# Optimization experiments

Hardware: AMD Instinct MI355X
Metric: run time of the kernel (lower is better)

Reference implementation:

```python
import jax, jax.numpy as jnp
from jax import lax
import numpy as np

B, S, T = 1024, 512, 48


def setup_inputs() -> dict:
    key = jax.random.key(0)
    k1, k2, k3, k4, k5, k6 = jax.random.split(key, 6)
    emissions = jax.random.normal(k1, (B, S, T), dtype=jnp.float32)
    tags = jax.random.randint(k2, (B, S), 0, T, dtype=jnp.int32)
    # variable-length mask; length >= 1 so position 0 is always valid
    lengths = jax.random.randint(k3, (B,), 1, S + 1, dtype=jnp.int32)
    mask = (jnp.arange(S)[None, :] < lengths[:, None]).astype(jnp.float32)
    transitions = jax.random.normal(k4, (T, T), dtype=jnp.float32)
    start_transitions = jax.random.normal(k5, (T,), dtype=jnp.float32)
    end_transitions = jax.random.normal(k6, (T,), dtype=jnp.float32)
    return {
        "emissions": emissions,
        "tags": tags,
        "mask": mask,
        "transitions": transitions,
        "start_transitions": start_transitions,
        "end_transitions": end_transitions,
    }


def _gold_score(emissions, tags, mask, transitions, start_transitions, end_transitions):
    # score of the gold tag sequence (vectorized over time)
    score = start_transitions[tags[:, 0]]
    score = score + jnp.take_along_axis(emissions[:, 0], tags[:, 0:1], axis=1)[:, 0]
    # NOTE: original code indexes transitions[cur_tag, prev_tag] here (faithful)
    trans_sc = transitions[tags[:, 1:], tags[:, :-1]]                      # [B, S-1]
    emit_sc = jnp.take_along_axis(emissions[:, 1:], tags[:, 1:, None], axis=2)[..., 0]
    score = score + jnp.sum((trans_sc + emit_sc) * mask[:, 1:], axis=1)
    seq_last = mask.sum(axis=1).astype(jnp.int32) - 1                      # [B]
    last_tags = jnp.take_along_axis(tags, seq_last[:, None], axis=1)[:, 0]
    return score + end_transitions[last_tags]


def _forward_algorithm(emissions, mask, transitions, start_transitions, end_transitions):
    # log-partition via logsumexp recurrence, lax.scan over time
    init = start_transitions[None, :] + emissions[:, 0]                    # [B, T]

    def step(score, xs):
        em_i, m_i = xs                                                     # [B,T], [B]
        # next[b, cur] = logsumexp_prev(score[b,prev] + trans[prev,cur] + em[b,cur])
        ns = jax.nn.logsumexp(score[:, :, None] + transitions[None] + em_i[:, None, :], axis=1)
        score = jnp.where(m_i[:, None] > 0, ns, score)
        return score, None

    xs = (jnp.swapaxes(emissions[:, 1:], 0, 1), jnp.swapaxes(mask[:, 1:], 0, 1))
    score, _ = lax.scan(step, init, xs)
    return jax.nn.logsumexp(score + end_transitions[None, :], axis=1)      # [B]


def reference(emissions, tags, mask, transitions, start_transitions, end_transitions):
    gold = _gold_score(emissions, tags, mask, transitions, start_transitions, end_transitions)
    fwd = _forward_algorithm(emissions, mask, transitions, start_transitions, end_transitions)
    return (fwd - gold).mean()
```

## Files before the change

### kernel.cpp

```cpp
#include <hip/hip_runtime.h>


#define T 48
#define SLEN 512
#define BATCH 1024

typedef _Float16 h2 __attribute__((ext_vector_type(2)));
typedef _Float16 h8v __attribute__((ext_vector_type(8)));
typedef h8v h8 __attribute__((may_alias));
typedef _Float16 f16ma __attribute__((may_alias));

__device__ __forceinline__ float wave_sum(float v) {
    #pragma unroll
    for (int m = 32; m >= 1; m >>= 1) v += __shfl_xor(v, m, 64);
    return v;
}
__device__ __forceinline__ float wave_max(float v) {
    #pragma unroll
    for (int m = 32; m >= 1; m >>= 1) v = fmaxf(v, __shfl_xor(v, m, 64));
    return v;
}
__device__ __forceinline__ float rlane(float v, int k) {
    return __int_as_float(__builtin_amdgcn_readlane(__float_as_int(v), k));
}
__device__ __forceinline__ float fdot2(h2 a, h2 b, float c) {
#if __has_builtin(__builtin_amdgcn_fdot2)
    return __builtin_amdgcn_fdot2(a, b, c, false);
#else
    return fmaf((float)a[1], (float)b[1], fmaf((float)a[0], (float)b[0], c));
#endif
}

#define H2OF(q, i) (__builtin_shufflevector((q), (q), 2*(i), 2*(i)+1))
#define DOTG(q, E, base, A0, A1, A2, A3)        \
    A0 = fdot2(H2OF(q,0), E[(base)+0], A0);     \
    A1 = fdot2(H2OF(q,1), E[(base)+1], A1);     \
    A2 = fdot2(H2OF(q,2), E[(base)+2], A2);     \
    A3 = fdot2(H2OF(q,3), E[(base)+3], A3);
#define DOT48(E, A0, A1, A2, A3, Q0,Q1,Q2,Q3,Q4,Q5) \
    DOTG(Q0, E, 0,  A0,A1,A2,A3)                \
    DOTG(Q1, E, 4,  A0,A1,A2,A3)                \
    DOTG(Q2, E, 8,  A0,A1,A2,A3)                \
    DOTG(Q3, E, 12, A0,A1,A2,A3)                \
    DOTG(Q4, E, 16, A0,A1,A2,A3)                \
    DOTG(Q5, E, 20, A0,A1,A2,A3)

__global__ __launch_bounds__(64) void crf_kernel(
    const float* __restrict__ em,
    const int*   __restrict__ tags,
    const float* __restrict__ mask,
    const float* __restrict__ trans,
    const float* __restrict__ start_t,
    const float* __restrict__ end_t,
    float*       __restrict__ out)
{
    constexpr float LOG2E = 1.4426950408889634f;
    constexpr float LN2   = 0.6931471805599453f;
    constexpr float ESC   = -8.0f;

    const int b    = blockIdx.x;
    const int lane = threadIdx.x;
    const int j    = lane < T ? lane : (T - 1);

    const float* em_b   = em   + (size_t)b * SLEN * T;
    const float* mask_b = mask + (size_t)b * SLEN;
    const int*   tags_b = tags + (size_t)b * SLEN;

    __shared__ __align__(16) _Float16 bufF[64];
    __shared__ __align__(16) _Float16 bufB[64];
    f16ma* wF = (f16ma*)bufF;
    f16ma* wB = (f16ma*)bufB;
    const h8* F8 = (const h8*)bufF;
    const h8* B8 = (const h8*)bufB;

    float msum = 0.f;
    for (int s = lane; s < SLEN; s += 64) msum += mask_b[s];
    msum = wave_sum(msum);
    const int len = (int)(msum + 0.5f);
    const int nb  = (len - 1) >> 1;
    const int nf  = (len - 1) - nb;

    float g = 0.f;
    for (int i = lane; i < len; i += 64) {
        if (i >= 1) {
            const int tc = tags_b[i];
            const int tp = tags_b[i - 1];
            g += trans[tc * T + tp] + em_b[(size_t)i * T + tc];
        }
    }
    g = wave_sum(g);

    h2 Ec[24], Er[24];
    #pragma unroll
    for (int k = 0; k < T; k += 2) {
        h2 c, r;
        c[0] = (_Float16)exp2f(trans[(k    ) * T + j] * LOG2E + ESC);
        c[1] = (_Float16)exp2f(trans[(k + 1) * T + j] * LOG2E + ESC);
        r[0] = (_Float16)exp2f(trans[j * T + (k    )] * LOG2E + ESC);
        r[1] = (_Float16)exp2f(trans[j * T + (k + 1)] * LOG2E + ESC);
        Ec[k >> 1] = c; Er[k >> 1] = r;
    }

    const float z0 = (start_t[j] + em_b[j]) * LOG2E;
    const float m0 = wave_max(z0);
    float pf = exp2f(z0 - m0);
    float u  = exp2f(end_t[j] * LOG2E);
    float Lf = m0, Lb = 0.f;

    const float* ep = em_b + j;
    const int maxoff = (SLEN - 1) * T;

    const float vlast  = ep[(size_t)(len - 1) * T];
    const float vextra = ep[(size_t)nf * T];

    wF[lane] = (_Float16)pf;
    wB[lane] = (_Float16)fminf(u * exp2f(vlast * LOG2E), 60000.f);
    h8 qF0=F8[0],qF1=F8[1],qF2=F8[2],qF3=F8[3],qF4=F8[4],qF5=F8[5];
    h8 qB0=B8[0],qB1=B8[1],qB2=B8[2],qB3=B8[3],qB4=B8[4],qB5=B8[5];

    int fo = T;
    float f0 = ep[fo < maxoff ? fo : maxoff]; fo += T;
    float f1 = ep[fo < maxoff ? fo : maxoff]; fo += T;
    float f2 = ep[fo < maxoff ? fo : maxoff]; fo += T;
    float f3 = ep[fo < maxoff ? fo : maxoff]; fo += T;
    int bo = (len - 2) * T;
    float e0 = ep[bo > 0 ? bo : 0]; bo -= T;
    float e1 = ep[bo > 0 ? bo : 0]; bo -= T;
    float e2 = ep[bo > 0 ? bo : 0]; bo -= T;
    float e3 = ep[bo > 0 ? bo : 0]; bo -= T;

    auto rescale = [&](float& v, float& L) {
        float m = fmaxf(fmaxf(rlane(v, 0), rlane(v, 16)),
                        fmaxf(rlane(v, 32), rlane(v, 47)));
        int e = ((__float_as_int(m) >> 23) & 255) - 127;
        e = e < -64 ? -64 : e;
        v *= __int_as_float((127 - e) << 23);
        L += (float)e;
    };

    auto jiter = [&](float& fe, float& be, bool resc) {
        float wf = exp2f(fe * LOG2E);
        fe = ep[fo < maxoff ? fo : maxoff]; fo += T;
        float a0=0.f, a1=0.f, a2=0.f, a3=0.f;
        DOT48(Ec, a0,a1,a2,a3, qF0,qF1,qF2,qF3,qF4,qF5)
        float pn = ((a0 + a1) + (a2 + a3)) * wf;
        if (resc) rescale(pn, Lf);
        pf = pn;
        wF[lane] = (_Float16)fminf(pn, 60000.f);
        qF0=F8[0];qF1=F8[1];qF2=F8[2];qF3=F8[3];qF4=F8[4];qF5=F8[5];
        float wb = exp2f(be * LOG2E);
        be = ep[bo > 0 ? bo : 0]; bo -= T;
        float c0=0.f, c1=0.f, c2=0.f, c3=0.f;
        DOT48(Er, c0,c1,c2,c3, qB0,qB1,qB2,qB3,qB4,qB5)
        float un = (c0 + c1) + (c2 + c3);
        if (resc) rescale(un, Lb);
        u = un;
        wB[lane] = (_Float16)fminf(un * wb, 60000.f);
        qB0=B8[0];qB1=B8[1];qB2=B8[2];qB3=B8[3];qB4=B8[4];qB5=B8[5];
    };

    int rem = nb;
    while (rem >= 4) {
        jiter(f0, e0, false);
        jiter(f1, e1, false);
        jiter(f2, e2, false);
        jiter(f3, e3, true);
        rem -= 4;
    }
    if (rem > 0) { jiter(f0, e0, false);
        if (rem > 1) { jiter(f1, e1, false);
            if (rem > 2) jiter(f2, e2, false); } }

    if (nf > nb) {
        float wf = exp2f(vextra * LOG2E);
        float a0=0.f, a1=0.f, a2=0.f, a3=0.f;
        DOT48(Ec, a0,a1,a2,a3, qF0,qF1,qF2,qF3,qF4,qF5)
        pf = ((a0 + a1) + (a2 + a3)) * wf;
    }

    Lf += 8.0f * (float)nf;
    Lb += 8.0f * (float)nb;
    const float v  = (lane < T) ? pf * u : 0.f;
    const float S_ = wave_sum(v);
    const float fwd = (Lf + Lb + log2f(S_)) * LN2;

    if (lane == 0) {
        const int t0 = tags_b[0];
        const int tl = tags_b[len - 1];
        const float gold = g + start_t[t0] + em_b[t0] + end_t[tl];
        atomicAdd(out, (fwd - gold) * (1.0f / (float)BATCH));
    }
}

extern "C" void kernel_launch(void* const* d_in, const int* in_sizes, int n_in,
                              void* d_out, int out_size, void* d_ws, size_t ws_size,
                              hipStream_t stream) {
    const float* em      = (const float*)d_in[0];
    const int*   tags    = (const int*)  d_in[1];
    const float* mask    = (const float*)d_in[2];
    const float* trans   = (const float*)d_in[3];
    const float* start_t = (const float*)d_in[4];
    const float* end_t   = (const float*)d_in[5];
    float* out = (float*)d_out;

    hipMemsetAsync(out, 0, sizeof(float), stream);
    crf_kernel<<<BATCH, 64, 0, stream>>>(em, tags, mask, trans, start_t, end_t, out);
}
```

Measured before the change: 210.6 us.

## Split forward and backward recurrences across wave halves, two tags per lane

New measurement: 210.6 us. Within noise of the previous version (-0.0%).

```diff
diff --git a/kernel.cpp b/kernel.cpp
--- a/kernel.cpp
+++ b/kernel.cpp
@@ -8,15 +8,15 @@
 typedef _Float16 h2 __attribute__((ext_vector_type(2)));
 typedef _Float16 h8v __attribute__((ext_vector_type(8)));
 typedef h8v h8 __attribute__((may_alias));
-typedef _Float16 f16ma __attribute__((may_alias));
+typedef h2 h2ma __attribute__((may_alias));
 
 __device__ __forceinline__ float wave_sum(float v) {
-    #pragma unroll
+#pragma unroll
     for (int m = 32; m >= 1; m >>= 1) v += __shfl_xor(v, m, 64);
     return v;
 }
 __device__ __forceinline__ float wave_max(float v) {
-    #pragma unroll
+#pragma unroll
     for (int m = 32; m >= 1; m >>= 1) v = fmaxf(v, __shfl_xor(v, m, 64));
     return v;
 }
@@ -32,18 +32,18 @@
 }
 
 #define H2OF(q, i) (__builtin_shufflevector((q), (q), 2*(i), 2*(i)+1))
-#define DOTG(q, E, base, A0, A1, A2, A3)        \
-    A0 = fdot2(H2OF(q,0), E[(base)+0], A0);     \
-    A1 = fdot2(H2OF(q,1), E[(base)+1], A1);     \
-    A2 = fdot2(H2OF(q,2), E[(base)+2], A2);     \
-    A3 = fdot2(H2OF(q,3), E[(base)+3], A3);
-#define DOT48(E, A0, A1, A2, A3, Q0,Q1,Q2,Q3,Q4,Q5) \
-    DOTG(Q0, E, 0,  A0,A1,A2,A3)                \
-    DOTG(Q1, E, 4,  A0,A1,A2,A3)                \
-    DOTG(Q2, E, 8,  A0,A1,A2,A3)                \
-    DOTG(Q3, E, 12, A0,A1,A2,A3)                \
-    DOTG(Q4, E, 16, A0,A1,A2,A3)                \
-    DOTG(Q5, E, 20, A0,A1,A2,A3)
+
+#define DG(qr, t)                              \
+    a0 = fdot2(H2OF(qr,0), EA[(t)+0], a0);     \
+    c0 = fdot2(H2OF(qr,0), EB[(t)+0], c0);     \
+    a1 = fdot2(H2OF(qr,1), EA[(t)+1], a1);     \
+    c1 = fdot2(H2OF(qr,1), EB[(t)+1], c1);     \
+    a2 = fdot2(H2OF(qr,2), EA[(t)+2], a2);     \
+    c2 = fdot2(H2OF(qr,2), EB[(t)+2], c2);     \
+    a3 = fdot2(H2OF(qr,3), EA[(t)+3], a3);     \
+    c3 = fdot2(H2OF(qr,3), EB[(t)+3], c3);
+
+#define DOT96() DG(q0,0) DG(q1,4) DG(q2,8) DG(q3,12) DG(q4,16) DG(q5,20)
 
 __global__ __launch_bounds__(64) void crf_kernel(
     const float* __restrict__ em,
@@ -58,20 +58,17 @@
     constexpr float LN2   = 0.6931471805599453f;
     constexpr float ESC   = -8.0f;
 
-    const int b    = blockIdx.x;
-    const int lane = threadIdx.x;
-    const int j    = lane < T ? lane : (T - 1);
+    const int  b    = blockIdx.x;
+    const int  lane = threadIdx.x;
+    const bool isF  = lane < 32;
+    const int  l31  = lane & 31;
+    const bool act  = l31 < 24;
+    const int  lc   = act ? l31 : 23;
+    const int  j0   = 2 * lc, j1 = j0 + 1;
 
     const float* em_b   = em   + (size_t)b * SLEN * T;
     const float* mask_b = mask + (size_t)b * SLEN;
     const int*   tags_b = tags + (size_t)b * SLEN;
-
-    __shared__ __align__(16) _Float16 bufF[64];
-    __shared__ __align__(16) _Float16 bufB[64];
-    f16ma* wF = (f16ma*)bufF;
-    f16ma* wB = (f16ma*)bufB;
-    const h8* F8 = (const h8*)bufF;
-    const h8* B8 = (const h8*)bufB;
 
     float msum = 0.f;
     for (int s = lane; s < SLEN; s += 64) msum += mask_b[s];
@@ -90,98 +87,119 @@
     }
     g = wave_sum(g);
 
-    h2 Ec[24], Er[24];
-    #pragma unroll
+    h2 EA[24], EB[24];
+#pragma unroll
     for (int k = 0; k < T; k += 2) {
-        h2 c, r;
-        c[0] = (_Float16)exp2f(trans[(k    ) * T + j] * LOG2E + ESC);
-        c[1] = (_Float16)exp2f(trans[(k + 1) * T + j] * LOG2E + ESC);
-        r[0] = (_Float16)exp2f(trans[j * T + (k    )] * LOG2E + ESC);
-        r[1] = (_Float16)exp2f(trans[j * T + (k + 1)] * LOG2E + ESC);
-        Ec[k >> 1] = c; Er[k >> 1] = r;
-    }
-
-    const float z0 = (start_t[j] + em_b[j]) * LOG2E;
-    const float m0 = wave_max(z0);
-    float pf = exp2f(z0 - m0);
-    float u  = exp2f(end_t[j] * LOG2E);
-    float Lf = m0, Lb = 0.f;
-
-    const float* ep = em_b + j;
+        const int iA0 = isF ? ((k    ) * T + j0) : (j0 * T + k    );
+        const int iA1 = isF ? ((k + 1) * T + j0) : (j0 * T + k + 1);
+        const int iB0 = isF ? ((k    ) * T + j1) : (j1 * T + k    );
+        const int iB1 = isF ? ((k + 1) * T + j1) : (j1 * T + k + 1);
+        h2 ea, eb;
+        ea[0] = (_Float16)exp2f(trans[iA0] * LOG2E + ESC);
+        ea[1] = (_Float16)exp2f(trans[iA1] * LOG2E + ESC);
+        eb[0] = (_Float16)exp2f(trans[iB0] * LOG2E + ESC);
+        eb[1] = (_Float16)exp2f(trans[iB1] * LOG2E + ESC);
+        EA[k >> 1] = ea; EB[k >> 1] = eb;
+    }
+
+    const float* ep2 = em_b + j0;
     const int maxoff = (SLEN - 1) * T;
-
-    const float vlast  = ep[(size_t)(len - 1) * T];
-    const float vextra = ep[(size_t)nf * T];
-
-    wF[lane] = (_Float16)pf;
-    wB[lane] = (_Float16)fminf(u * exp2f(vlast * LOG2E), 60000.f);
-    h8 qF0=F8[0],qF1=F8[1],qF2=F8[2],qF3=F8[3],qF4=F8[4],qF5=F8[5];
-    h8 qB0=B8[0],qB1=B8[1],qB2=B8[2],qB3=B8[3],qB4=B8[4],qB5=B8[5];
-
-    int fo = T;
-    float f0 = ep[fo < maxoff ? fo : maxoff]; fo += T;
-    float f1 = ep[fo < maxoff ? fo : maxoff]; fo += T;
-    float f2 = ep[fo < maxoff ? fo : maxoff]; fo += T;
-    float f3 = ep[fo < maxoff ? fo : maxoff]; fo += T;
-    int bo = (len - 2) * T;
-    float e0 = ep[bo > 0 ? bo : 0]; bo -= T;
-    float e1 = ep[bo > 0 ? bo : 0]; bo -= T;
-    float e2 = ep[bo > 0 ? bo : 0]; bo -= T;
-    float e3 = ep[bo > 0 ? bo : 0]; bo -= T;
-
-    auto rescale = [&](float& v, float& L) {
-        float m = fmaxf(fmaxf(rlane(v, 0), rlane(v, 16)),
-                        fmaxf(rlane(v, 32), rlane(v, 47)));
-        int e = ((__float_as_int(m) >> 23) & 255) - 127;
-        e = e < -64 ? -64 : e;
-        v *= __int_as_float((127 - e) << 23);
-        L += (float)e;
+    const float2 vlast2  = *(const float2*)(ep2 + (size_t)(len - 1) * T);
+    const float2 vextra2 = *(const float2*)(ep2 + (size_t)nf * T);
+
+    const float za = (start_t[j0] + em_b[j0]) * LOG2E;
+    const float zb = (start_t[j1] + em_b[j1]) * LOG2E;
+    const float m0 = wave_max(isF ? fmaxf(za, zb) : -1e30f);
+    float st0, st1, L;
+    if (isF) {
+        st0 = exp2f(za - m0); st1 = exp2f(zb - m0); L = m0;
+    } else {
+        st0 = exp2f(end_t[j0] * LOG2E);
+        st1 = exp2f(end_t[j1] * LOG2E);
+        L = 0.f;
+    }
+
+    __shared__ __align__(16) _Float16 sh[128];
+    {
+        const float w0 = exp2f(vlast2.x * LOG2E);
+        const float w1 = exp2f(vlast2.y * LOG2E);
+        h2 p;
+        p[0] = (_Float16)(isF ? st0 : fminf(st0 * w0, 60000.f));
+        p[1] = (_Float16)(isF ? st1 : fminf(st1 * w1, 60000.f));
+        *(h2ma*)&sh[2 * lane] = p;
+    }
+    const h8* Qb = (const h8*)(sh + ((lane & 32) << 1));
+    h8 q0 = {}, q1 = {}, q2 = {}, q3 = {}, q4 = {}, q5 = {};
+    if (act) { q0 = Qb[0]; q1 = Qb[1]; q2 = Qb[2]; q3 = Qb[3]; q4 = Qb[4]; q5 = Qb[5]; }
+
+    const int dlt = isF ? T : -T;
+    int off = isF ? T : (len - 2) * T;
+    auto ldem = [&]() -> float2 {
+        int oc = off;
+        oc = oc < 0 ? 0 : oc;
+        oc = oc > maxoff ? maxoff : oc;
+        const float2 r = *(const float2*)(ep2 + oc);
+        off += dlt;
+        return r;
     };
-
-    auto jiter = [&](float& fe, float& be, bool resc) {
-        float wf = exp2f(fe * LOG2E);
-        fe = ep[fo < maxoff ? fo : maxoff]; fo += T;
-        float a0=0.f, a1=0.f, a2=0.f, a3=0.f;
-        DOT48(Ec, a0,a1,a2,a3, qF0,qF1,qF2,qF3,qF4,qF5)
-        float pn = ((a0 + a1) + (a2 + a3)) * wf;
-        if (resc) rescale(pn, Lf);
-        pf = pn;
-        wF[lane] = (_Float16)fminf(pn, 60000.f);
-        qF0=F8[0];qF1=F8[1];qF2=F8[2];qF3=F8[3];qF4=F8[4];qF5=F8[5];
-        float wb = exp2f(be * LOG2E);
-        be = ep[bo > 0 ? bo : 0]; bo -= T;
-        float c0=0.f, c1=0.f, c2=0.f, c3=0.f;
-        DOT48(Er, c0,c1,c2,c3, qB0,qB1,qB2,qB3,qB4,qB5)
-        float un = (c0 + c1) + (c2 + c3);
-        if (resc) rescale(un, Lb);
-        u = un;
-        wB[lane] = (_Float16)fminf(un * wb, 60000.f);
-        qB0=B8[0];qB1=B8[1];qB2=B8[2];qB3=B8[3];qB4=B8[4];qB5=B8[5];
+    float2 r0 = ldem(), r1 = ldem(), r2 = ldem(), r3 = ldem();
+
+    auto jiter = [&](float2& slot, bool resc) {
+        const float w0 = exp2f(slot.x * LOG2E);
+        const float w1 = exp2f(slot.y * LOG2E);
+        slot = ldem();
+        float a0=0.f,a1=0.f,a2=0.f,a3=0.f,c0=0.f,c1=0.f,c2=0.f,c3=0.f;
+        DOT96()
+        float s0 = (a0 + a1) + (a2 + a3);
+        float s1 = (c0 + c1) + (c2 + c3);
+        if (isF) { s0 *= w0; s1 *= w1; }
+        if (resc) {
+            const float m  = fmaxf(s0, s1);
+            const float mf = fmaxf(fmaxf(rlane(m, 0),  rlane(m, 8)),
+                                   fmaxf(rlane(m, 16), rlane(m, 23)));
+            const float mb = fmaxf(fmaxf(rlane(m, 32), rlane(m, 40)),
+                                   fmaxf(rlane(m, 48), rlane(m, 55)));
+            int e = ((__float_as_int(isF ? mf : mb) >> 23) & 255) - 127;
+            e = e < -64 ? -64 : e;
+            const float sc = __int_as_float((127 - e) << 23);
+            s0 *= sc; s1 *= sc; L += (float)e;
+        }
+        st0 = s0; st1 = s1;
+        h2 p;
+        p[0] = (_Float16)fminf(isF ? s0 : s0 * w0, 60000.f);
+        p[1] = (_Float16)fminf(isF ? s1 : s1 * w1, 60000.f);
+        *(h2ma*)&sh[2 * lane] = p;
+        if (act) { q0 = Qb[0]; q1 = Qb[1]; q2 = Qb[2]; q3 = Qb[3]; q4 = Qb[4]; q5 = Qb[5]; }
     };
 
     int rem = nb;
     while (rem >= 4) {
-        jiter(f0, e0, false);
-        jiter(f1, e1, false);
-        jiter(f2, e2, false);
-        jiter(f3, e3, true);
+        jiter(r0, false); jiter(r1, false); jiter(r2, false); jiter(r3, true);
         rem -= 4;
     }
-    if (rem > 0) { jiter(f0, e0, false);
-        if (rem > 1) { jiter(f1, e1, false);
-            if (rem > 2) jiter(f2, e2, false); } }
+    if (rem > 0) { jiter(r0, false);
+        if (rem > 1) { jiter(r1, false);
+            if (rem > 2) jiter(r2, false); } }
+
+    L += 8.0f * (float)(isF ? nf : nb);
 
     if (nf > nb) {
-        float wf = exp2f(vextra * LOG2E);
-        float a0=0.f, a1=0.f, a2=0.f, a3=0.f;
-        DOT48(Ec, a0,a1,a2,a3, qF0,qF1,qF2,qF3,qF4,qF5)
-        pf = ((a0 + a1) + (a2 + a3)) * wf;
-    }
-
-    Lf += 8.0f * (float)nf;
-    Lb += 8.0f * (float)nb;
-    const float v  = (lane < T) ? pf * u : 0.f;
+        const float w0 = exp2f(vextra2.x * LOG2E);
+        const float w1 = exp2f(vextra2.y * LOG2E);
+        float a0=0.f,a1=0.f,a2=0.f,a3=0.f,c0=0.f,c1=0.f,c2=0.f,c3=0.f;
+        DOT96()
+        if (isF) {
+            st0 = ((a0 + a1) + (a2 + a3)) * w0;
+            st1 = ((c0 + c1) + (c2 + c3)) * w1;
+        }
+    }
+
+    const float u0 = __shfl_xor(st0, 32, 64);
+    const float u1 = __shfl_xor(st1, 32, 64);
+    const float v  = (isF && act) ? (st0 * u0 + st1 * u1) : 0.f;
     const float S_ = wave_sum(v);
+    const float Lf = rlane(L, 0);
+    const float Lb = rlane(L, 32);
     const float fwd = (Lf + Lb + log2f(S_)) * LN2;
 
     if (lane == 0) {
```
